# Kernel optimization log

Hardware: AMD Instinct MI355X
Metric: run time of the kernel (lower is better)

Reference implementation:

```python
import jax, jax.numpy as jnp
import numpy as np

DEPTH = 6
IN_FEATURES = 256
NUM_TREES = 256
TREE_DIM = 1
BATCH = 2048


def sparsemax(X, axis=0):
    """Full-sort sparsemax projection along `axis` (k=None path of the torch code)."""
    X = jnp.moveaxis(X, axis, -1)
    Xs = X - jnp.max(X, axis=-1, keepdims=True)
    z = -jnp.sort(-Xs, axis=-1)                      # descending sort
    cs = jnp.cumsum(z, axis=-1) - 1.0                # topk_cumsum - 1
    d = X.shape[-1]
    rho = jnp.arange(1, d + 1, dtype=X.dtype)
    support = rho * z > cs
    k = jnp.sum(support, axis=-1, keepdims=True)     # support size (int)
    tau = jnp.take_along_axis(cs, k - 1, axis=-1) / k.astype(X.dtype)
    out = jnp.maximum(Xs - tau, 0.0)
    return jnp.moveaxis(out, -1, axis)


def sparsemoid(x):
    return jnp.clip(0.5 * x + 0.5, 0.0, 1.0)


def bin_codes_1hot(depth, dtype=jnp.float32):
    idx = jnp.arange(2 ** depth)
    off = 2 ** jnp.arange(depth)
    codes = ((idx[None, :] // off[:, None]) % 2).astype(dtype)   # [depth, 2^depth]
    return jnp.stack([codes, 1.0 - codes], axis=-1)              # [depth, 2^depth, 2]


def setup_inputs() -> dict:
    key = jax.random.key(0)
    k1, k2, k3, k4, k5 = jax.random.split(key, 5)
    x = jax.random.normal(k1, (BATCH, IN_FEATURES), dtype=jnp.float32)
    response = jax.random.normal(k2, (NUM_TREES, TREE_DIM, 2 ** DEPTH), dtype=jnp.float32)
    feature_selection_logits = jax.random.uniform(k3, (IN_FEATURES, NUM_TREES, DEPTH), dtype=jnp.float32)
    feature_thresholds = 0.5 * jax.random.normal(k4, (NUM_TREES, DEPTH), dtype=jnp.float32)
    log_temperatures = jnp.zeros((NUM_TREES, DEPTH), dtype=jnp.float32)
    return {
        "x": x,
        "response": response,
        "feature_selection_logits": feature_selection_logits,
        "feature_thresholds": feature_thresholds,
        "log_temperatures": log_temperatures,
    }


def reference(x, response, feature_selection_logits, feature_thresholds, log_temperatures):
    depth = feature_thresholds.shape[-1]
    codes = bin_codes_1hot(depth, x.dtype)                          # [d, 2^d, 2]
    # sparsemax feature routing over the feature axis
    fs = sparsemax(feature_selection_logits, axis=0)                # [F, T, d]
    fv = jnp.einsum('bi,ind->bnd', x, fs)                           # [B, T, d]
    tl = (fv - feature_thresholds) * jnp.exp(-log_temperatures)     # [B, T, d]
    bins = sparsemoid(jnp.stack([-tl, tl], axis=-1))                # [B, T, d, 2]
    bin_matches = jnp.einsum('btds,dcs->btdc', bins, codes)         # [B, T, d, 2^d]
    response_weights = jnp.prod(bin_matches, axis=-2)               # [B, T, 2^d]
    out = jnp.einsum('bnd,ncd->bnc', response_weights, response)    # [B, T, C]
    return out.reshape(out.shape[0], -1)                            # flatten_output=True
```

## Files before the change

### kernel.cpp

```cpp
#include <hip/hip_runtime.h>
#include <math.h>

#define NF 256
#define NT 256
#define ND 6
#define NB 2048
#define NCOL (NT * ND)
#define NLEAF 64

typedef __attribute__((ext_vector_type(8))) short bf16x8;
typedef __attribute__((ext_vector_type(4))) float f32x4;
typedef __attribute__((ext_vector_type(8))) unsigned short u16x8;

__device__ inline unsigned short f2bf(float f) {
    unsigned u = __float_as_uint(f);
    u += 0x7fffu + ((u >> 16) & 1u);
    return (unsigned short)(u >> 16);
}
__device__ inline float bf2f(unsigned short h) {
    return __uint_as_float(((unsigned)h) << 16);
}

__global__ __launch_bounds__(256) void sparsemax_michelot(
    const float* __restrict__ fsl,
    unsigned short* __restrict__ fs_hi,
    unsigned short* __restrict__ fs_lo)
{
    const int lane = threadIdx.x & 63;
    const int col  = blockIdx.x * 4 + (threadIdx.x >> 6);

    float x[4];
    #pragma unroll
    for (int j = 0; j < 4; j++)
        x[j] = fsl[(lane + 64 * j) * NCOL + col];

    float mx = fmaxf(fmaxf(x[0], x[1]), fmaxf(x[2], x[3]));
    #pragma unroll
    for (int off = 32; off > 0; off >>= 1)
        mx = fmaxf(mx, __shfl_xor(mx, off));
    #pragma unroll
    for (int j = 0; j < 4; j++) x[j] -= mx;

    float s = (x[0] + x[1]) + (x[2] + x[3]);
    #pragma unroll
    for (int off = 32; off > 0; off >>= 1)
        s += __shfl_xor(s, off);
    float tau = (s - 1.0f) / 256.0f;

    int prev = 256;
    for (int it = 0; it < 64; it++) {
        float ss = 0.0f, cc = 0.0f;
        #pragma unroll
        for (int j = 0; j < 4; j++)
            if (x[j] > tau) { ss += x[j]; cc += 1.0f; }
        #pragma unroll
        for (int off = 32; off > 0; off >>= 1) {
            ss += __shfl_xor(ss, off);
            cc += __shfl_xor(cc, off);
        }
        const int c = (int)cc;
        if (c == prev) break;
        prev = c;
        tau = (ss - 1.0f) / cc;
    }

    #pragma unroll
    for (int j = 0; j < 4; j++) {
        const float v = fmaxf(x[j] - tau, 0.0f);
        const unsigned short h = f2bf(v);
        fs_hi[col * NF + lane + 64 * j] = h;
        fs_lo[col * NF + lane + 64 * j] = f2bf(v - bf2f(h));
    }
}

#define TM 64
#define TN 96
#define TK 32
#define PK (TK + 8)

union SMem {
    struct {
        unsigned short Ah[TM][PK], Al[TM][PK];
        unsigned short Bh[TN][PK], Bl[TN][PK];
    } st;
    struct {
        float fv[TM][TN + 1];
        float resp[16][NLEAF];
    } ep;
};

__global__ __launch_bounds__(256) void gemm_tree_kernel(
    const float* __restrict__ x,
    const unsigned short* __restrict__ Bh,
    const unsigned short* __restrict__ Bl,
    const float* __restrict__ thr,
    const float* __restrict__ ltemp,
    const float* __restrict__ resp_g,
    float* __restrict__ out)
{
    __shared__ SMem sm;

    const int tid  = threadIdx.x;
    const int lane = tid & 63;
    const int w    = tid >> 6;
    const int wm   = w & 1;
    const int wn   = w >> 1;
    const int bm0  = blockIdx.y * TM;
    const int bn0  = blockIdx.x * TN;
    const int t0   = blockIdx.x * 16;

    const int l15  = lane & 15;
    const int quad = lane >> 4;

    const int arow  = tid >> 2;
    const int akseg = (tid & 3) * 8;
    const int bhalf = tid >> 7;
    const int brow  = (tid & 127) >> 2;
    const int bkseg = (tid & 3) * 8;

    f32x4 acc[2][3] = {};

    for (int k0 = 0; k0 < NF; k0 += TK) {
        {
            const float4 v0 = *(const float4*)&x[(bm0 + arow) * NF + k0 + akseg];
            const float4 v1 = *(const float4*)&x[(bm0 + arow) * NF + k0 + akseg + 4];
            const float vv[8] = {v0.x, v0.y, v0.z, v0.w, v1.x, v1.y, v1.z, v1.w};
            u16x8 hi, lo;
            #pragma unroll
            for (int j = 0; j < 8; j++) {
                const unsigned short h = f2bf(vv[j]);
                hi[j] = h;
                lo[j] = f2bf(vv[j] - bf2f(h));
            }
            *(u16x8*)&sm.st.Ah[arow][akseg] = hi;
            *(u16x8*)&sm.st.Al[arow][akseg] = lo;
        }
        {
            const unsigned short* __restrict__ src = bhalf ? Bl : Bh;
            unsigned short (*dst)[PK] = bhalf ? sm.st.Bl : sm.st.Bh;
            #pragma unroll
            for (int c = 0; c < 3; c++) {
                const int row = c * 32 + brow;
                *(u16x8*)&dst[row][bkseg] =
                    *(const u16x8*)&src[(bn0 + row) * NF + k0 + bkseg];
            }
        }
        __syncthreads();

        #pragma unroll
        for (int im = 0; im < 2; im++) {
            const bf16x8 a_h = *(const bf16x8*)&sm.st.Ah[wm * 32 + im * 16 + l15][quad * 8];
            const bf16x8 a_l = *(const bf16x8*)&sm.st.Al[wm * 32 + im * 16 + l15][quad * 8];
            #pragma unroll
            for (int in = 0; in < 3; in++) {
                const bf16x8 b_h = *(const bf16x8*)&sm.st.Bh[wn * 48 + in * 16 + l15][quad * 8];
                const bf16x8 b_l = *(const bf16x8*)&sm.st.Bl[wn * 48 + in * 16 + l15][quad * 8];
                acc[im][in] = __builtin_amdgcn_mfma_f32_16x16x32_bf16(a_h, b_h, acc[im][in], 0, 0, 0);
                acc[im][in] = __builtin_amdgcn_mfma_f32_16x16x32_bf16(a_h, b_l, acc[im][in], 0, 0, 0);
                acc[im][in] = __builtin_amdgcn_mfma_f32_16x16x32_bf16(a_l, b_h, acc[im][in], 0, 0, 0);
            }
        }
        __syncthreads();
    }

    #pragma unroll
    for (int im = 0; im < 2; im++)
        #pragma unroll
        for (int in = 0; in < 3; in++)
            #pragma unroll
            for (int r = 0; r < 4; r++) {
                const int m = wm * 32 + im * 16 + quad * 4 + r;
                const int n = wn * 48 + in * 16 + l15;
                sm.ep.fv[m][n] = acc[im][in][r];
            }
    {
        const int tr  = tid >> 4;
        const int seg = (tid & 15) * 4;
        *(float4*)&sm.ep.resp[tr][seg] = *(const float4*)&resp_g[(t0 + tr) * NLEAF + seg];
    }
    __syncthreads();

    #pragma unroll
    for (int i = 0; i < 4; i++) {
        const int item = tid + 256 * i;
        const int m    = item & 63;
        const int t16  = item >> 6;
        const int t    = t0 + t16;

        float sp[ND], sn[ND];
        #pragma unroll
        for (int d = 0; d < ND; d++) {
            const float f  = sm.ep.fv[m][t16 * ND + d];
            const float tl = (f - thr[t * ND + d]) * __expf(-ltemp[t * ND + d]);
            const float h  = 0.5f * tl;
            sp[d] = fminf(fmaxf(0.5f + h, 0.0f), 1.0f);
            sn[d] = fminf(fmaxf(0.5f - h, 0.0f), 1.0f);
        }

        float wleaf[NLEAF];
        wleaf[0] = 1.0f;
        #pragma unroll
        for (int d = 0; d < ND; d++) {
            const int half = 1 << d;
            #pragma unroll
            for (int c = 0; c < NLEAF / 2; c++) {
                if (c < half) {
                    const float base = wleaf[c];
                    wleaf[c + half] = base * sn[d];
                    wleaf[c]        = base * sp[d];
                }
            }
        }

        float a = 0.0f;
        #pragma unroll
        for (int c = 0; c < NLEAF; c++)
            a = fmaf(wleaf[c], sm.ep.resp[t16][c], a);

        out[(bm0 + m) * NT + t] = a;
    }
}

extern "C" void kernel_launch(void* const* d_in, const int* in_sizes, int n_in,
                              void* d_out, int out_size, void* d_ws, size_t ws_size,
                              hipStream_t stream)
{
    const float* x    = (const float*)d_in[0];
    const float* resp = (const float*)d_in[1];
    const float* fsl  = (const float*)d_in[2];
    const float* thr  = (const float*)d_in[3];
    const float* lt   = (const float*)d_in[4];
    float* out = (float*)d_out;

    unsigned short* fs_hi = (unsigned short*)d_ws;
    unsigned short* fs_lo = fs_hi + (size_t)NCOL * NF;

    sparsemax_michelot<<<NCOL / 4, 256, 0, stream>>>(fsl, fs_hi, fs_lo);

    dim3 g(NCOL / TN, NB / TM);
    gemm_tree_kernel<<<g, 256, 0, stream>>>(x, fs_hi, fs_lo, thr, lt, resp, out);
}
```

Baseline: 89.83 us.

## Pre-split x to bf16 hi/lo, double-buffer GEMM with direct-to-LDS loads

The setup kernel now also splits x into bf16 hi/lo arrays and precomputes exp(-log_temperature), so the GEMM no longer converts x on every tile. The GEMM main loop uses global_load_lds into two XOR-swizzled LDS buffers, so the next K tile loads while the current one runs MFMAs. The epilogue stages thresholds and scales in shared memory and replaces building the 64 leaf weights with a folded reduction over the response vector. This adds workspace traffic for the x copies, and there is only one barrier per iteration, which could be a race risk.

```diff
diff --git a/kernel.cpp b/kernel.cpp
--- a/kernel.cpp
+++ b/kernel.cpp
@@ -1,5 +1,6 @@
 #include <hip/hip_runtime.h>
 #include <math.h>
+#include <stdint.h>
 
 #define NF 256
 #define NT 256
@@ -10,7 +11,7 @@
 
 typedef __attribute__((ext_vector_type(8))) short bf16x8;
 typedef __attribute__((ext_vector_type(4))) float f32x4;
-typedef __attribute__((ext_vector_type(8))) unsigned short u16x8;
+typedef __attribute__((ext_vector_type(4))) unsigned short u16x4;
 
 __device__ inline unsigned short f2bf(float f) {
     unsigned u = __float_as_uint(f);
@@ -21,27 +22,40 @@
     return __uint_as_float(((unsigned)h) << 16);
 }
 
-__global__ __launch_bounds__(256) void sparsemax_michelot(
+__device__ inline void gld16(const void* g, void* l) {
+    __builtin_amdgcn_global_load_lds(
+        (const __attribute__((address_space(1))) unsigned int*)(uintptr_t)g,
+        (__attribute__((address_space(3))) unsigned int*)(uintptr_t)l,
+        16, 0, 0);
+}
+
+__global__ __launch_bounds__(256) void setup_kernel(
     const float* __restrict__ fsl,
+    const float* __restrict__ x,
+    const float* __restrict__ lt,
     unsigned short* __restrict__ fs_hi,
-    unsigned short* __restrict__ fs_lo)
+    unsigned short* __restrict__ fs_lo,
+    unsigned short* __restrict__ x_hi,
+    unsigned short* __restrict__ x_lo,
+    float* __restrict__ scl)
 {
-    const int lane = threadIdx.x & 63;
-    const int col  = blockIdx.x * 4 + (threadIdx.x >> 6);
-
-    float x[4];
+    const int tid  = threadIdx.x;
+    const int lane = tid & 63;
+    const int col  = blockIdx.x * 4 + (tid >> 6);
+
+    float xv[4];
     #pragma unroll
     for (int j = 0; j < 4; j++)
-        x[j] = fsl[(lane + 64 * j) * NCOL + col];
-
-    float mx = fmaxf(fmaxf(x[0], x[1]), fmaxf(x[2], x[3]));
+        xv[j] = fsl[(lane + 64 * j) * NCOL + col];
+
+    float mx = fmaxf(fmaxf(xv[0], xv[1]), fmaxf(xv[2], xv[3]));
     #pragma unroll
     for (int off = 32; off > 0; off >>= 1)
         mx = fmaxf(mx, __shfl_xor(mx, off));
     #pragma unroll
-    for (int j = 0; j < 4; j++) x[j] -= mx;
-
-    float s = (x[0] + x[1]) + (x[2] + x[3]);
+    for (int j = 0; j < 4; j++) xv[j] -= mx;
+
+    float s = (xv[0] + xv[1]) + (xv[2] + xv[3]);
     #pragma unroll
     for (int off = 32; off > 0; off >>= 1)
         s += __shfl_xor(s, off);
@@ -52,7 +66,7 @@
         float ss = 0.0f, cc = 0.0f;
         #pragma unroll
         for (int j = 0; j < 4; j++)
-            if (x[j] > tau) { ss += x[j]; cc += 1.0f; }
+            if (xv[j] > tau) { ss += xv[j]; cc += 1.0f; }
         #pragma unroll
         for (int off = 32; off > 0; off >>= 1) {
             ss += __shfl_xor(ss, off);
@@ -66,35 +80,57 @@
 
     #pragma unroll
     for (int j = 0; j < 4; j++) {
-        const float v = fmaxf(x[j] - tau, 0.0f);
+        const float v = fmaxf(xv[j] - tau, 0.0f);
         const unsigned short h = f2bf(v);
         fs_hi[col * NF + lane + 64 * j] = h;
         fs_lo[col * NF + lane + 64 * j] = f2bf(v - bf2f(h));
     }
+
+    const int gid = blockIdx.x * 256 + tid;
+    for (int e = gid; e < NB * NF / 4; e += (NCOL / 4) * 256) {
+        const float4 v = ((const float4*)x)[e];
+        const float vv[4] = {v.x, v.y, v.z, v.w};
+        u16x4 h, l;
+        #pragma unroll
+        for (int j = 0; j < 4; j++) {
+            h[j] = f2bf(vv[j]);
+            l[j] = f2bf(vv[j] - bf2f(h[j]));
+        }
+        ((u16x4*)x_hi)[e] = h;
+        ((u16x4*)x_lo)[e] = l;
+    }
+
+    if (gid < NT * ND) scl[gid] = __expf(-lt[gid]);
 }
 
 #define TM 64
 #define TN 96
 #define TK 32
-#define PK (TK + 8)
+
+struct MainBuf {
+    unsigned short Ah[TM * TK];
+    unsigned short Al[TM * TK];
+    unsigned short Bh[TN * TK];
+    unsigned short Bl[TN * TK];
+};
 
 union SMem {
-    struct {
-        unsigned short Ah[TM][PK], Al[TM][PK];
-        unsigned short Bh[TN][PK], Bl[TN][PK];
-    } st;
+    MainBuf mb[2];
     struct {
         float fv[TM][TN + 1];
-        float resp[16][NLEAF];
+        float resp[16][NLEAF + 4];
+        float th[16 * ND];
+        float sc[16 * ND];
     } ep;
 };
 
 __global__ __launch_bounds__(256) void gemm_tree_kernel(
-    const float* __restrict__ x,
-    const unsigned short* __restrict__ Bh,
-    const unsigned short* __restrict__ Bl,
+    const unsigned short* __restrict__ x_hi,
+    const unsigned short* __restrict__ x_lo,
+    const unsigned short* __restrict__ fs_hi,
+    const unsigned short* __restrict__ fs_lo,
     const float* __restrict__ thr,
-    const float* __restrict__ ltemp,
+    const float* __restrict__ scl,
     const float* __restrict__ resp_g,
     float* __restrict__ out)
 {
@@ -112,49 +148,60 @@
     const int l15  = lane & 15;
     const int quad = lane >> 4;
 
-    const int arow  = tid >> 2;
-    const int akseg = (tid & 3) * 8;
-    const int bhalf = tid >> 7;
-    const int brow  = (tid & 127) >> 2;
-    const int bkseg = (tid & 3) * 8;
+    const int lr = lane >> 2;
+    const int cp = lane & 3;
+
+    const int rA  = (w << 4) + lr;
+    const int cA  = cp ^ ((rA >> 1) & 3);
+    const unsigned short* pAh = x_hi + (bm0 + rA) * NF + cA * 8;
+    const unsigned short* pAl = x_lo + (bm0 + rA) * NF + cA * 8;
+
+    const int s0  = w;
+    const int rB0 = (s0 << 4) + lr;
+    const int cB0 = cp ^ ((rB0 >> 1) & 3);
+    const unsigned short* pBh0 = fs_hi + (bn0 + rB0) * NF + cB0 * 8;
+    const unsigned short* pBl0 = fs_lo + (bn0 + rB0) * NF + cB0 * 8;
+    const int s1  = w + 4;
+    const int rB1 = (s1 << 4) + lr;
+    const int cB1 = cp ^ ((rB1 >> 1) & 3);
+    const unsigned short* pBh1 = fs_hi + (bn0 + rB1) * NF + cB1 * 8;
+    const unsigned short* pBl1 = fs_lo + (bn0 + rB1) * NF + cB1 * 8;
+
+    auto stage = [&](int kb, int k0) {
+        MainBuf& b = sm.mb[kb];
+        gld16(pAh + k0, &b.Ah[w << 9]);
+        gld16(pAl + k0, &b.Al[w << 9]);
+        gld16(pBh0 + k0, &b.Bh[s0 << 9]);
+        gld16(pBl0 + k0, &b.Bl[s0 << 9]);
+        if (w < 2) {
+            gld16(pBh1 + k0, &b.Bh[s1 << 9]);
+            gld16(pBl1 + k0, &b.Bl[s1 << 9]);
+        }
+    };
 
     f32x4 acc[2][3] = {};
 
-    for (int k0 = 0; k0 < NF; k0 += TK) {
-        {
-            const float4 v0 = *(const float4*)&x[(bm0 + arow) * NF + k0 + akseg];
-            const float4 v1 = *(const float4*)&x[(bm0 + arow) * NF + k0 + akseg + 4];
-            const float vv[8] = {v0.x, v0.y, v0.z, v0.w, v1.x, v1.y, v1.z, v1.w};
-            u16x8 hi, lo;
-            #pragma unroll
-            for (int j = 0; j < 8; j++) {
-                const unsigned short h = f2bf(vv[j]);
-                hi[j] = h;
-                lo[j] = f2bf(vv[j] - bf2f(h));
-            }
-            *(u16x8*)&sm.st.Ah[arow][akseg] = hi;
-            *(u16x8*)&sm.st.Al[arow][akseg] = lo;
-        }
-        {
-            const unsigned short* __restrict__ src = bhalf ? Bl : Bh;
-            unsigned short (*dst)[PK] = bhalf ? sm.st.Bl : sm.st.Bh;
-            #pragma unroll
-            for (int c = 0; c < 3; c++) {
-                const int row = c * 32 + brow;
-                *(u16x8*)&dst[row][bkseg] =
-                    *(const u16x8*)&src[(bn0 + row) * NF + k0 + bkseg];
-            }
-        }
-        __syncthreads();
-
+    stage(0, 0);
+    __syncthreads();
+
+    #pragma unroll
+    for (int t = 0; t < NF / TK; ++t) {
+        const int kb = t & 1;
+        if (t < NF / TK - 1) stage(kb ^ 1, (t + 1) * TK);
+
+        MainBuf& b = sm.mb[kb];
         #pragma unroll
         for (int im = 0; im < 2; im++) {
-            const bf16x8 a_h = *(const bf16x8*)&sm.st.Ah[wm * 32 + im * 16 + l15][quad * 8];
-            const bf16x8 a_l = *(const bf16x8*)&sm.st.Al[wm * 32 + im * 16 + l15][quad * 8];
+            const int ar = wm * 32 + im * 16 + l15;
+            const int sa = (quad ^ ((ar >> 1) & 3)) * 8;
+            const bf16x8 a_h = *(const bf16x8*)&b.Ah[ar * TK + sa];
+            const bf16x8 a_l = *(const bf16x8*)&b.Al[ar * TK + sa];
             #pragma unroll
             for (int in = 0; in < 3; in++) {
-                const bf16x8 b_h = *(const bf16x8*)&sm.st.Bh[wn * 48 + in * 16 + l15][quad * 8];
-                const bf16x8 b_l = *(const bf16x8*)&sm.st.Bl[wn * 48 + in * 16 + l15][quad * 8];
+                const int br = wn * 48 + in * 16 + l15;
+                const int sb = (quad ^ ((br >> 1) & 3)) * 8;
+                const bf16x8 b_h = *(const bf16x8*)&b.Bh[br * TK + sb];
+                const bf16x8 b_l = *(const bf16x8*)&b.Bl[br * TK + sb];
                 acc[im][in] = __builtin_amdgcn_mfma_f32_16x16x32_bf16(a_h, b_h, acc[im][in], 0, 0, 0);
                 acc[im][in] = __builtin_amdgcn_mfma_f32_16x16x32_bf16(a_h, b_l, acc[im][in], 0, 0, 0);
                 acc[im][in] = __builtin_amdgcn_mfma_f32_16x16x32_bf16(a_l, b_h, acc[im][in], 0, 0, 0);
@@ -176,48 +223,41 @@
     {
         const int tr  = tid >> 4;
         const int seg = (tid & 15) * 4;
-        *(float4*)&sm.ep.resp[tr][seg] = *(const float4*)&resp_g[(t0 + tr) * NLEAF + seg];
-    }
+        *(f32x4*)&sm.ep.resp[tr][seg] = *(const f32x4*)&resp_g[(t0 + tr) * NLEAF + seg];
+    }
+    if (tid < 16 * ND)       sm.ep.th[tid]      = thr[t0 * ND + tid];
+    else if (tid < 32 * ND)  sm.ep.sc[tid - 96] = scl[t0 * ND + tid - 96];
     __syncthreads();
 
+    const int t16 = tid & 15;
+    const int mr  = tid >> 4;
     #pragma unroll
     for (int i = 0; i < 4; i++) {
-        const int item = tid + 256 * i;
-        const int m    = item & 63;
-        const int t16  = item >> 6;
-        const int t    = t0 + t16;
+        const int m = mr + 16 * i;
 
         float sp[ND], sn[ND];
         #pragma unroll
         for (int d = 0; d < ND; d++) {
             const float f  = sm.ep.fv[m][t16 * ND + d];
-            const float tl = (f - thr[t * ND + d]) * __expf(-ltemp[t * ND + d]);
+            const float tl = (f - sm.ep.th[t16 * ND + d]) * sm.ep.sc[t16 * ND + d];
             const float h  = 0.5f * tl;
             sp[d] = fminf(fmaxf(0.5f + h, 0.0f), 1.0f);
             sn[d] = fminf(fmaxf(0.5f - h, 0.0f), 1.0f);
         }
 
-        float wleaf[NLEAF];
-        wleaf[0] = 1.0f;
-        #pragma unroll
-        for (int d = 0; d < ND; d++) {
+        float r[32];
+        #pragma unroll
+        for (int c = 0; c < 32; c++)
+            r[c] = sp[5] * sm.ep.resp[t16][c] + sn[5] * sm.ep.resp[t16][c + 32];
+        #pragma unroll
+        for (int d = 4; d >= 0; d--) {
             const int half = 1 << d;
             #pragma unroll
-            for (int c = 0; c < NLEAF / 2; c++) {
-                if (c < half) {
-                    const float base = wleaf[c];
-                    wleaf[c + half] = base * sn[d];
-                    wleaf[c]        = base * sp[d];
-                }
-            }
-        }
-
-        float a = 0.0f;
-        #pragma unroll
-        for (int c = 0; c < NLEAF; c++)
-            a = fmaf(wleaf[c], sm.ep.resp[t16][c], a);
-
-        out[(bm0 + m) * NT + t] = a;
+            for (int c = 0; c < 32; c++)
+                if (c < half) r[c] = sp[d] * r[c] + sn[d] * r[c + half];
+        }
+
+        out[(bm0 + m) * NT + t0 + t16] = r[0];
     }
 }
 
@@ -234,9 +274,12 @@
 
     unsigned short* fs_hi = (unsigned short*)d_ws;
     unsigned short* fs_lo = fs_hi + (size_t)NCOL * NF;
-
-    sparsemax_michelot<<<NCOL / 4, 256, 0, stream>>>(fsl, fs_hi, fs_lo);
+    unsigned short* x_hi  = fs_lo + (size_t)NCOL * NF;
+    unsigned short* x_lo  = x_hi + (size_t)NB * NF;
+    float*          scl   = (float*)(x_lo + (size_t)NB * NF);
+
+    setup_kernel<<<NCOL / 4, 256, 0, stream>>>(fsl, x, lt, fs_hi, fs_lo, x_hi, x_lo, scl);
 
     dim3 g(NCOL / TN, NB / TM);
-    gemm_tree_kernel<<<g, 256, 0, stream>>>(x, fs_hi, fs_lo, thr, lt, resp, out);
-}
+    gemm_tree_kernel<<<g, 256, 0, stream>>>(x_hi, x_lo, fs_hi, fs_lo, thr, scl, resp, out);
+}
```

After: 95.60 us. 6.4% more time.
